# Optimization experiments

Hardware: AMD Instinct MI355X
Metric: run time of the kernel (lower is better)

The kernel has to match this reference:

```python
import jax, jax.numpy as jnp
import numpy as np

N_NODES = 50000
N_EDGES = 1_600_000
NFEAT = 512
NHID = 256  # nhid*2 = 512, nhid*3 = 768
NCLASS = 64
H2, H3 = 2 * NHID, 3 * NHID


def _uniform(key, shape, stdv):
    return jax.random.uniform(key, shape, jnp.float32, -stdv, stdv)


def setup_inputs() -> dict:
    key = jax.random.key(0)
    ks = jax.random.split(key, 16)
    x = jax.random.normal(ks[0], (N_NODES, NFEAT), jnp.float32)
    adj_row = jax.random.randint(ks[1], (N_EDGES,), 0, N_NODES, jnp.int64 if jax.config.jax_enable_x64 else jnp.int32)
    adj_col = jax.random.randint(ks[2], (N_EDGES,), 0, N_NODES, jnp.int64 if jax.config.jax_enable_x64 else jnp.int32)
    adj_val = jax.random.uniform(ks[3], (N_EDGES,), jnp.float32)
    # nn.Linear init: U(-1/sqrt(fan_in), 1/sqrt(fan_in)); GraphConvolution: U(-1/sqrt(out), 1/sqrt(out))
    s_org = 1.0 / np.sqrt(NFEAT)
    s_gc1 = 1.0 / np.sqrt(H3)
    s_gc2 = 1.0 / np.sqrt(H3)
    s_l3 = 1.0 / np.sqrt(H2)
    s_out = 1.0 / np.sqrt(H3)
    return {
        "x": x, "adj_row": adj_row, "adj_col": adj_col, "adj_val": adj_val,
        "W_org": _uniform(ks[4], (NFEAT, H2), s_org), "b_org": _uniform(ks[5], (H2,), s_org),
        "W_gc1": _uniform(ks[6], (H2, H3), s_gc1), "b_gc1": _uniform(ks[7], (H3,), s_gc1),
        "W_gc2": _uniform(ks[8], (H3, H3), s_gc2), "b_gc2": _uniform(ks[9], (H3,), s_gc2),
        "W_l3": _uniform(ks[10], (H2, H3), s_l3), "b_l3": _uniform(ks[11], (H3,), s_l3),
        "W_out": _uniform(ks[12], (H3, NCLASS), s_out), "b_out": _uniform(ks[13], (NCLASS,), s_out),
    }


def _spmm(row, col, val, dense):
    # out[i] = sum_{e: row[e]==i} val[e] * dense[col[e]]
    msgs = val[:, None] * dense[col]            # [E, F] gather + scale
    return jax.ops.segment_sum(msgs, row, num_segments=N_NODES)


def reference(x, adj_row, adj_col, adj_val,
              W_org, b_org, W_gc1, b_gc1, W_gc2, b_gc2,
              W_l3, b_l3, W_out, b_out):
    # linear_org (dropout = identity in eval)
    h = x @ W_org + b_org                       # [N, H2]
    # GCN layer 1: mm then spmm, bias, relu
    g = _spmm(adj_row, adj_col, adj_val, h @ W_gc1) + b_gc1
    g = jax.nn.relu(g)
    # GCN layer 2
    g = _spmm(adj_row, adj_col, adj_val, g @ W_gc2) + b_gc2
    # residual mix + output head
    z = (h @ W_l3 + b_l3) + 0.5 * g             # [N, H3]
    out = z @ W_out + b_out                     # [N, NCLASS]
    # global min-max normalization to [-1, 1]
    mn, mx = jnp.min(out), jnp.max(out)
    return 2.0 * (out - mn) / (mx - mn) - 1.0
```

## Files before the change

kernel.cpp:

```cpp
#include <hip/hip_runtime.h>

#define N_NODES 50000
#define N_EDGES 1600000
#define NFEAT   512
#define H2      512
#define H3      768
#define NCLASS  64
#define E_CAP   (N_EDGES + 8 * N_NODES)

typedef __attribute__((ext_vector_type(8))) short bf16x8;
typedef __attribute__((ext_vector_type(4))) float f32x4;
typedef __attribute__((ext_vector_type(8))) _Float16 f16x8;
typedef __attribute__((ext_vector_type(8))) unsigned short u16x8;

__device__ __forceinline__ unsigned short f2bf(float f) {
    unsigned u = __builtin_bit_cast(unsigned, f);
    unsigned r = (u + 0x7FFF + ((u >> 16) & 1)) >> 16;
    return (unsigned short)r;
}
__device__ __forceinline__ float bf2f(unsigned short h) {
    unsigned u = ((unsigned)h) << 16;
    return __builtin_bit_cast(float, u);
}

__device__ __forceinline__ void gload_lds16(const void* g, void* l) {
    __builtin_amdgcn_global_load_lds(
        (const __attribute__((address_space(1))) void*)g,
        (__attribute__((address_space(3))) void*)l, 16, 0, 0);
}

__global__ __launch_bounds__(256) void fold_weights_kernel(
    const float* __restrict__ Wgc2, const float* __restrict__ Wl3,
    const float* __restrict__ Wout, const float* __restrict__ b_gc2,
    const float* __restrict__ b_l3, const float* __restrict__ b_out,
    float* __restrict__ Wco, float* __restrict__ Wlo, float* __restrict__ bias_total)
{
    const int b = blockIdx.x;
    const int tid = threadIdx.x;
    if (b < 192) {
        int elem = b * 256 + tid;
        int r = elem >> 6, c = elem & 63;
        float s = 0.f;
        for (int k = 0; k < H3; ++k)
            s = fmaf(Wgc2[r * H3 + k], Wout[k * NCLASS + c], s);
        Wco[elem] = s;
    } else if (b < 320) {
        int elem = (b - 192) * 256 + tid;
        int r = elem >> 6, c = elem & 63;
        float s = 0.f;
        for (int k = 0; k < H3; ++k)
            s = fmaf(Wl3[r * H3 + k], Wout[k * NCLASS + c], s);
        Wlo[elem] = s;
    } else {
        if (tid < NCLASS) {
            float s = b_out[tid];
            for (int k = 0; k < H3; ++k)
                s = fmaf(b_l3[k] + 0.5f * b_gc2[k], Wout[k * NCLASS + tid], s);
            bias_total[tid] = s;
        }
    }
}

__global__ __launch_bounds__(256) void prep_weights_kernel(
    const float* __restrict__ Worg, const float* __restrict__ Wgc1,
    const float* __restrict__ Wco, const float* __restrict__ Wlo,
    unsigned short* __restrict__ WorgT_hi, unsigned short* __restrict__ WorgT_lo,
    unsigned short* __restrict__ Wgc1T_hi, unsigned short* __restrict__ Wgc1T_lo,
    unsigned short* __restrict__ WcoT_hi,  unsigned short* __restrict__ WcoT_lo,
    unsigned short* __restrict__ WloT_hi,  unsigned short* __restrict__ WloT_lo)
{
    int e = blockIdx.x * 256 + threadIdx.x;
    float v; unsigned short* hi; unsigned short* lo; int idx;
    if (e < 262144) {
        int n = e >> 9, k = e & 511;
        v = Worg[k * H2 + n]; hi = WorgT_hi; lo = WorgT_lo; idx = e;
    } else if (e < 262144 + 393216) {
        int e2 = e - 262144;
        int n = e2 >> 9, k = e2 & 511;
        v = Wgc1[k * H3 + n]; hi = Wgc1T_hi; lo = Wgc1T_lo; idx = e2;
    } else if (e < 262144 + 393216 + 49152) {
        int e3 = e - 262144 - 393216;
        int n = e3 / H3, k = e3 % H3;
        v = Wco[k * NCLASS + n]; hi = WcoT_hi; lo = WcoT_lo; idx = e3;
    } else if (e < 262144 + 393216 + 49152 + 32768) {
        int e4 = e - 262144 - 393216 - 49152;
        int n = e4 >> 9, k = e4 & 511;
        v = Wlo[k * NCLASS + n]; hi = WloT_hi; lo = WloT_lo; idx = e4;
    } else return;
    unsigned short hv = f2bf(v);
    hi[idx] = hv;
    lo[idx] = f2bf(v - bf2f(hv));
}

__global__ __launch_bounds__(256) void hist_kernel(const int* __restrict__ rows,
                                                   int* __restrict__ counts)
{
    int e = blockIdx.x * 256 + threadIdx.x;
    if (e < N_EDGES) atomicAdd(&counts[rows[e]], 1);
}

__global__ __launch_bounds__(256) void scan_blocks_kernel(
    const int* __restrict__ counts, int* __restrict__ row_ptr,
    int* __restrict__ btot, int n)
{
    __shared__ int wsum[4];
    const int idx = blockIdx.x * 256 + threadIdx.x;
    const int lane = threadIdx.x & 63;
    const int wid  = threadIdx.x >> 6;
    int v = (idx < n) ? ((counts[idx] + 7) & ~7) : 0;
    int x = v;
    #pragma unroll
    for (int off = 1; off < 64; off <<= 1) {
        int y = __shfl_up(x, off, 64);
        if (lane >= off) x += y;
    }
    if (lane == 63) wsum[wid] = x;
    __syncthreads();
    if (threadIdx.x == 0) {
        int s = 0;
        #pragma unroll
        for (int i = 0; i < 4; ++i) { int t = wsum[i]; wsum[i] = s; s += t; }
        btot[blockIdx.x] = s;
    }
    __syncthreads();
    if (idx < n) row_ptr[idx] = x - v + wsum[wid];
}

__global__ __launch_bounds__(256) void scan_tots_kernel(int* __restrict__ btot, int nb)
{
    __shared__ int wsum[4];
    const int tid = threadIdx.x;
    const int lane = tid & 63;
    const int wid  = tid >> 6;
    int v = (tid < nb) ? btot[tid] : 0;
    int x = v;
    #pragma unroll
    for (int off = 1; off < 64; off <<= 1) {
        int y = __shfl_up(x, off, 64);
        if (lane >= off) x += y;
    }
    if (lane == 63) wsum[wid] = x;
    __syncthreads();
    if (tid == 0) {
        int s = 0;
        #pragma unroll
        for (int i = 0; i < 4; ++i) { int t = wsum[i]; wsum[i] = s; s += t; }
    }
    __syncthreads();
    int excl = x - v + wsum[wid];
    if (tid < nb) btot[tid] = excl;
    if (tid == nb - 1) btot[nb] = excl + v;
}

__global__ __launch_bounds__(256) void scan_add_kernel(
    const int* __restrict__ btot, int* __restrict__ row_ptr,
    int* __restrict__ row_cur, int n)
{
    int idx = blockIdx.x * 256 + threadIdx.x;
    if (idx < n) {
        int o = row_ptr[idx] + btot[blockIdx.x];
        row_ptr[idx] = o;
        row_cur[idx] = o;
    }
    if (idx == 0) row_ptr[n] = btot[gridDim.x];
}

__global__ __launch_bounds__(256) void scatter_kernel(
    const int* __restrict__ rows, const int* __restrict__ cols,
    const float* __restrict__ vals, int* __restrict__ row_cur,
    int* __restrict__ cols_s, float* __restrict__ vals_s)
{
    int e = blockIdx.x * 256 + threadIdx.x;
    if (e < N_EDGES) {
        int r = rows[e];
        int p = atomicAdd(&row_cur[r], 1);
        cols_s[p] = cols[e];
        vals_s[p] = vals[e];
    }
}

template <int BN, int EPI, int AMODE, int WMODE>
__global__ __launch_bounds__(256, 2) void gemm_mfma(
    const float* __restrict__ Af, const _Float16* __restrict__ Ah16,
    const unsigned short* __restrict__ Ahi, const unsigned short* __restrict__ Alo,
    const unsigned short* __restrict__ Bhi, const unsigned short* __restrict__ Blo,
    const float* __restrict__ bias, const float* __restrict__ extra,
    float* __restrict__ Cf, _Float16* __restrict__ Ch16,
    unsigned short* __restrict__ Chi, unsigned short* __restrict__ Clo,
    int M, int N, int K, int NB)
{
    constexpr int WNF = BN / 32;
    constexpr int BF  = BN / 16;
    constexpr int NCH = 16 + 2 * BF;
    __shared__ unsigned short lds[NCH * 512];

    const int tid  = threadIdx.x;
    const int lane = tid & 63;
    const int wid  = tid >> 6;
    const int wr   = wid >> 1, wc = wid & 1;
    const int fr   = lane & 15;
    const int fk   = (lane >> 4) * 8;

    const int nwg = gridDim.x;
    const int u = blockIdx.x;
    const int q = nwg >> 3, r = nwg & 7;
    const int xcd = u & 7, pos = u >> 3;
    const int wg = (xcd < r ? xcd * (q + 1) : r * (q + 1) + (xcd - r) * q) + pos;
    const int m0 = (wg / NB) * 128;
    const int n0 = (wg % NB) * BN;

    f32x4 acc[4][WNF];
    #pragma unroll
    for (int mi = 0; mi < 4; ++mi)
        #pragma unroll
        for (int ni = 0; ni < WNF; ++ni)
            acc[mi][ni] = (f32x4){0.f, 0.f, 0.f, 0.f};

    for (int kt = 0; kt < K; kt += 32) {
        if constexpr (AMODE != 0) {
            #pragma unroll
            for (int sub = wid; sub < 8; sub += 4) {
                int row = m0 + sub * 16 + fr;
                if (row >= M) row = M - 1;
                float v[8];
                if constexpr (AMODE == 1) {
                    const float* src = Af + (size_t)row * K + kt + fk;
                    float4 p0 = *(const float4*)src;
                    float4 p1 = *(const float4*)(src + 4);
                    v[0] = p0.x; v[1] = p0.y; v[2] = p0.z; v[3] = p0.w;
                    v[4] = p1.x; v[5] = p1.y; v[6] = p1.z; v[7] = p1.w;
                } else {
                    const _Float16* src = Ah16 + (size_t)row * K + kt + fk;
                    f16x8 p = *(const f16x8*)src;
                    #pragma unroll
                    for (int j = 0; j < 8; ++j) v[j] = (float)p[j];
                }
                bf16x8 h8, l8;
                #pragma unroll
                for (int j = 0; j < 8; ++j) {
                    unsigned short hv = f2bf(v[j]);
                    h8[j] = (short)hv;
                    l8[j] = (short)f2bf(v[j] - bf2f(hv));
                }
                *(bf16x8*)&lds[sub * 512 + lane * 8] = h8;
                *(bf16x8*)&lds[(8 + sub) * 512 + lane * 8] = l8;
            }
            for (int ch = 16 + wid; ch < NCH; ch += 4) {
                int bch = ch - 16;
                int sub = bch % BF;
                const unsigned short* base = (bch < BF) ? Bhi : Blo;
                int col = n0 + sub * 16 + fr;
                gload_lds16(base + (size_t)col * K + kt + fk, &lds[ch * 512]);
            }
        } else {
            for (int ch = wid; ch < NCH; ch += 4) {
                const unsigned short* src;
                if (ch < 16) {
                    int sub = ch & 7;
                    int row = m0 + sub * 16 + fr;
                    if (row >= M) row = M - 1;
                    const unsigned short* base = (ch < 8) ? Ahi : Alo;
                    src = base + (size_t)row * K + kt + fk;
                } else {
                    int bch = ch - 16;
                    int sub = bch % BF;
                    const unsigned short* base = (bch < BF) ? Bhi : Blo;
                    int col = n0 + sub * 16 + fr;
                    src = base + (size_t)col * K + kt + fk;
                }
                gload_lds16(src, &lds[ch * 512]);
            }
        }
        __syncthreads();

        bf16x8 ah[4], al[4], bh[WNF], bl[WNF];
        #pragma unroll
        for (int mi = 0; mi < 4; ++mi) {
            int mf = wr * 4 + mi;
            ah[mi] = *(const bf16x8*)&lds[mf * 512 + lane * 8];
            al[mi] = *(const bf16x8*)&lds[(8 + mf) * 512 + lane * 8];
        }
        #pragma unroll
        for (int ni = 0; ni < WNF; ++ni) {
            int nf = wc * WNF + ni;
            bh[ni] = *(const bf16x8*)&lds[(16 + nf) * 512 + lane * 8];
            bl[ni] = *(const bf16x8*)&lds[(16 + BF + nf) * 512 + lane * 8];
        }
        #pragma unroll
        for (int mi = 0; mi < 4; ++mi)
            #pragma unroll
            for (int ni = 0; ni < WNF; ++ni) {
                acc[mi][ni] = __builtin_amdgcn_mfma_f32_16x16x32_bf16(
                    ah[mi], bh[ni], acc[mi][ni], 0, 0, 0);
                acc[mi][ni] = __builtin_amdgcn_mfma_f32_16x16x32_bf16(
                    ah[mi], bl[ni], acc[mi][ni], 0, 0, 0);
                acc[mi][ni] = __builtin_amdgcn_mfma_f32_16x16x32_bf16(
                    al[mi], bh[ni], acc[mi][ni], 0, 0, 0);
            }
        __syncthreads();
    }

    const int r0 = m0 + wr * 64 + (lane >> 4) * 4;
    const int c0 = n0 + wc * (BN / 2) + (lane & 15);
    #pragma unroll
    for (int mi = 0; mi < 4; ++mi)
        #pragma unroll
        for (int ni = 0; ni < WNF; ++ni) {
            int col = c0 + ni * 16;
            float bv = 0.f;
            if constexpr (EPI > 0) bv = bias[col];
            #pragma unroll
            for (int qi = 0; qi < 4; ++qi) {
                int row = r0 + mi * 16 + qi;
                if (row >= M) continue;
                float v = acc[mi][ni][qi] + bv;
                if constexpr (EPI == 2) v = fmaxf(v, 0.f);
                if constexpr (EPI == 3)
                    v = fmaf(0.5f, extra[(size_t)row * N + col], v);
                size_t idx = (size_t)row * N + col;
                if constexpr (WMODE == 0) Cf[idx] = v;
                if constexpr (WMODE == 1) {
                    unsigned short hv = f2bf(v);
                    Chi[idx] = hv;
                    Clo[idx] = f2bf(v - bf2f(hv));
                }
                if constexpr (WMODE == 2) Ch16[idx] = (_Float16)v;
            }
        }
}

__global__ __launch_bounds__(256) void spmm_csr512_f16(
    const int* __restrict__ row_ptr, const int* __restrict__ cols,
    const float* __restrict__ vals, const _Float16* __restrict__ dense,
    unsigned short* __restrict__ out_hi, unsigned short* __restrict__ out_lo)
{
    const int row = blockIdx.x * 4 + (threadIdx.x >> 6);
    const int c8 = (threadIdx.x & 63) * 8;
    int e = row_ptr[row];
    const int e1 = row_ptr[row + 1];
    float acc[8] = {0.f, 0.f, 0.f, 0.f, 0.f, 0.f, 0.f, 0.f};
    for (; e < e1; e += 8) {
        int4   ca = *(const int4*)&cols[e];
        int4   cb = *(const int4*)&cols[e + 4];
        float4 va = *(const float4*)&vals[e];
        float4 vb = *(const float4*)&vals[e + 4];
        f16x8 d0 = *(const f16x8*)&dense[(size_t)ca.x * 512 + c8];
        f16x8 d1 = *(const f16x8*)&dense[(size_t)ca.y * 512 + c8];
        f16x8 d2 = *(const f16x8*)&dense[(size_t)ca.z * 512 + c8];
        f16x8 d3 = *(const f16x8*)&dense[(size_t)ca.w * 512 + c8];
        f16x8 d4 = *(const f16x8*)&dense[(size_t)cb.x * 512 + c8];
        f16x8 d5 = *(const f16x8*)&dense[(size_t)cb.y * 512 + c8];
        f16x8 d6 = *(const f16x8*)&dense[(size_t)cb.z * 512 + c8];
        f16x8 d7 = *(const f16x8*)&dense[(size_t)cb.w * 512 + c8];
        #pragma unroll
        for (int j = 0; j < 8; ++j) {
            float a = acc[j];
            a = fmaf(va.x, (float)d0[j], a);
            a = fmaf(va.y, (float)d1[j], a);
            a = fmaf(va.z, (float)d2[j], a);
            a = fmaf(va.w, (float)d3[j], a);
            a = fmaf(vb.x, (float)d4[j], a);
            a = fmaf(vb.y, (float)d5[j], a);
            a = fmaf(vb.z, (float)d6[j], a);
            a = fmaf(vb.w, (float)d7[j], a);
            acc[j] = a;
        }
    }
    u16x8 h8, l8;
    #pragma unroll
    for (int j = 0; j < 8; ++j) {
        unsigned short hv = f2bf(acc[j]);
        h8[j] = hv;
        l8[j] = f2bf(acc[j] - bf2f(hv));
    }
    *(u16x8*)&out_hi[(size_t)row * 512 + c8] = h8;
    *(u16x8*)&out_lo[(size_t)row * 512 + c8] = l8;
}

__global__ __launch_bounds__(256) void spmm_csr64(
    const int* __restrict__ row_ptr, const int* __restrict__ cols,
    const float* __restrict__ vals, const float* __restrict__ dense,
    float* __restrict__ out)
{
    const int row = blockIdx.x * 4 + (threadIdx.x >> 6);
    const int c = threadIdx.x & 63;
    int e = row_ptr[row];
    const int e1 = row_ptr[row + 1];
    float a0 = 0.f, a1 = 0.f, a2 = 0.f, a3 = 0.f;
    for (; e < e1; e += 4) {
        int c0 = cols[e], c1 = cols[e + 1], c2 = cols[e + 2], c3 = cols[e + 3];
        float v0 = vals[e], v1 = vals[e + 1], v2 = vals[e + 2], v3 = vals[e + 3];
        a0 = fmaf(v0, dense[(size_t)c0 * 64 + c], a0);
        a1 = fmaf(v1, dense[(size_t)c1 * 64 + c], a1);
        a2 = fmaf(v2, dense[(size_t)c2 * 64 + c], a2);
        a3 = fmaf(v3, dense[(size_t)c3 * 64 + c], a3);
    }
    out[(size_t)row * 64 + c] = (a0 + a1) + (a2 + a3);
}

__global__ __launch_bounds__(256) void minmax_partial(const float* __restrict__ x,
                                                      int n, float* __restrict__ part)
{
    float mn = 3.4e38f, mx = -3.4e38f;
    for (int i = blockIdx.x * 256 + threadIdx.x; i < n; i += gridDim.x * 256) {
        float v = x[i];
        mn = fminf(mn, v); mx = fmaxf(mx, v);
    }
    #pragma unroll
    for (int off = 32; off > 0; off >>= 1) {
        mn = fminf(mn, __shfl_down(mn, off, 64));
        mx = fmaxf(mx, __shfl_down(mx, off, 64));
    }
    __shared__ float smn[4], smx[4];
    if ((threadIdx.x & 63) == 0) { smn[threadIdx.x >> 6] = mn; smx[threadIdx.x >> 6] = mx; }
    __syncthreads();
    if (threadIdx.x == 0) {
        mn = fminf(fminf(smn[0], smn[1]), fminf(smn[2], smn[3]));
        mx = fmaxf(fmaxf(smx[0], smx[1]), fmaxf(smx[2], smx[3]));
        part[blockIdx.x] = mn;
        part[gridDim.x + blockIdx.x] = mx;
    }
}

__global__ __launch_bounds__(256) void minmax_final(const float* __restrict__ part,
                                                    float* __restrict__ mm)
{
    float mn = part[threadIdx.x], mx = part[256 + threadIdx.x];
    #pragma unroll
    for (int off = 32; off > 0; off >>= 1) {
        mn = fminf(mn, __shfl_down(mn, off, 64));
        mx = fmaxf(mx, __shfl_down(mx, off, 64));
    }
    __shared__ float smn[4], smx[4];
    if ((threadIdx.x & 63) == 0) { smn[threadIdx.x >> 6] = mn; smx[threadIdx.x >> 6] = mx; }
    __syncthreads();
    if (threadIdx.x == 0) {
        mm[0] = fminf(fminf(smn[0], smn[1]), fminf(smn[2], smn[3]));
        mm[1] = fmaxf(fmaxf(smx[0], smx[1]), fmaxf(smx[2], smx[3]));
    }
}

__global__ __launch_bounds__(256) void normalize_kernel(float4* __restrict__ x, int n4,
                                                        const float* __restrict__ mm)
{
    int i = blockIdx.x * 256 + threadIdx.x;
    if (i >= n4) return;
    float mn = mm[0];
    float s = 2.0f / (mm[1] - mn);
    float4 v = x[i];
    v.x = fmaf(v.x - mn, s, -1.f);
    v.y = fmaf(v.y - mn, s, -1.f);
    v.z = fmaf(v.z - mn, s, -1.f);
    v.w = fmaf(v.w - mn, s, -1.f);
    x[i] = v;
}

extern "C" void kernel_launch(void* const* d_in, const int* in_sizes, int n_in,
                              void* d_out, int out_size, void* d_ws, size_t ws_size,
                              hipStream_t stream)
{
    const float* x       = (const float*)d_in[0];
    const int*   adj_row = (const int*)d_in[1];
    const int*   adj_col = (const int*)d_in[2];
    const float* adj_val = (const float*)d_in[3];
    const float* W_org = (const float*)d_in[4];
    const float* b_org = (const float*)d_in[5];
    const float* W_gc1 = (const float*)d_in[6];
    const float* b_gc1 = (const float*)d_in[7];
    const float* W_gc2 = (const float*)d_in[8];
    const float* b_gc2 = (const float*)d_in[9];
    const float* W_l3  = (const float*)d_in[10];
    const float* b_l3  = (const float*)d_in[11];
    const float* W_out = (const float*)d_in[12];
    const float* b_out = (const float*)d_in[13];
    float* out = (float*)d_out;

    char* w = (char*)d_ws;
    size_t off = 0;
    auto alloc = [&](size_t bytes) -> void* {
        void* p = w + off;
        off += (bytes + 255) & ~(size_t)255;
        return p;
    };
    unsigned short* g_hi = (unsigned short*)alloc((size_t)N_NODES * H3 * 2);
    unsigned short* g_lo = (unsigned short*)alloc((size_t)N_NODES * H3 * 2);
    _Float16* h16 = (_Float16*)alloc((size_t)N_NODES * H2 * 2);
    char* region_ah = (char*)alloc((size_t)N_NODES * H2 * 4);
    unsigned short* ah_hi = (unsigned short*)region_ah;
    unsigned short* ah_lo = ah_hi + (size_t)N_NODES * H2;
    float* s   = (float*)region_ah;
    float* as_ = s + (size_t)N_NODES * NCLASS;
    int*   counts  = (int*)alloc((size_t)N_NODES * 4);
    int*   row_ptr = (int*)alloc((size_t)(N_NODES + 1) * 4);
    int*   row_cur = (int*)alloc((size_t)N_NODES * 4);
    int*   btot    = (int*)alloc(256 * 4);
    int*   cols_s  = (int*)alloc((size_t)E_CAP * 4);
    float* vals_s  = (float*)alloc((size_t)E_CAP * 4);
    float* Wco = (float*)alloc((size_t)H3 * NCLASS * 4);
    float* Wlo = (float*)alloc((size_t)H2 * NCLASS * 4);
    unsigned short* WorgT_hi = (unsigned short*)alloc((size_t)H2 * NFEAT * 2);
    unsigned short* WorgT_lo = (unsigned short*)alloc((size_t)H2 * NFEAT * 2);
    unsigned short* Wgc1T_hi = (unsigned short*)alloc((size_t)H3 * H2 * 2);
    unsigned short* Wgc1T_lo = (unsigned short*)alloc((size_t)H3 * H2 * 2);
    unsigned short* WcoT_hi  = (unsigned short*)alloc((size_t)NCLASS * H3 * 2);
    unsigned short* WcoT_lo  = (unsigned short*)alloc((size_t)NCLASS * H3 * 2);
    unsigned short* WloT_hi  = (unsigned short*)alloc((size_t)NCLASS * H2 * 2);
    unsigned short* WloT_lo  = (unsigned short*)alloc((size_t)NCLASS * H2 * 2);
    float* bias_total = (float*)alloc(NCLASS * 4);
    float* part = (float*)alloc(512 * 4);
    float* mm   = (float*)alloc(2 * 4);
    (void)ws_size; (void)n_in; (void)in_sizes; (void)out_size;

    hipMemsetAsync(counts, 0, (size_t)N_NODES * 4, stream);
    hipMemsetAsync(cols_s, 0, (size_t)E_CAP * 4, stream);
    hipMemsetAsync(vals_s, 0, (size_t)E_CAP * 4, stream);
    fold_weights_kernel<<<321, 256, 0, stream>>>(W_gc2, W_l3, W_out, b_gc2, b_l3,
                                                 b_out, Wco, Wlo, bias_total);
    prep_weights_kernel<<<2880, 256, 0, stream>>>(W_org, W_gc1, Wco, Wlo,
        WorgT_hi, WorgT_lo, Wgc1T_hi, Wgc1T_lo, WcoT_hi, WcoT_lo, WloT_hi, WloT_lo);
    hist_kernel<<<N_EDGES / 256, 256, 0, stream>>>(adj_row, counts);
    const int NSB = (N_NODES + 255) / 256;
    scan_blocks_kernel<<<NSB, 256, 0, stream>>>(counts, row_ptr, btot, N_NODES);
    scan_tots_kernel<<<1, 256, 0, stream>>>(btot, NSB);
    scan_add_kernel<<<NSB, 256, 0, stream>>>(btot, row_ptr, row_cur, N_NODES);
    scatter_kernel<<<N_EDGES / 256, 256, 0, stream>>>(adj_row, adj_col, adj_val,
                                                      row_cur, cols_s, vals_s);

    const int MB = (N_NODES + 127) / 128;

    gemm_mfma<128, 1, 1, 2><<<MB * 4, 256, 0, stream>>>(
        x, nullptr, nullptr, nullptr, WorgT_hi, WorgT_lo, b_org, nullptr,
        nullptr, h16, nullptr, nullptr, N_NODES, H2, NFEAT, 4);
    spmm_csr512_f16<<<N_NODES / 4, 256, 0, stream>>>(row_ptr, cols_s, vals_s, h16,
                                                     ah_hi, ah_lo);
    gemm_mfma<128, 2, 0, 1><<<MB * 6, 256, 0, stream>>>(
        nullptr, nullptr, ah_hi, ah_lo, Wgc1T_hi, Wgc1T_lo, b_gc1, nullptr,
        nullptr, nullptr, g_hi, g_lo, N_NODES, H3, H2, 6);
    gemm_mfma<64, 0, 0, 0><<<MB, 256, 0, stream>>>(
        nullptr, nullptr, g_hi, g_lo, WcoT_hi, WcoT_lo, nullptr, nullptr,
        s, nullptr, nullptr, nullptr, N_NODES, NCLASS, H3, 1);
    spmm_csr64<<<N_NODES / 4, 256, 0, stream>>>(row_ptr, cols_s, vals_s, s, as_);
    gemm_mfma<64, 3, 2, 0><<<MB, 256, 0, stream>>>(
        nullptr, h16, nullptr, nullptr, WloT_hi, WloT_lo, bias_total, as_,
        out, nullptr, nullptr, nullptr, N_NODES, NCLASS, H2, 1);

    const int n_out = N_NODES * NCLASS;
    minmax_partial<<<256, 256, 0, stream>>>(out, n_out, part);
    minmax_final<<<1, 256, 0, stream>>>(part, mm);
    normalize_kernel<<<(n_out / 4 + 255) / 256, 256, 0, stream>>>(
        (float4*)out, n_out / 4, mm);
}
```

Measured before the change: 1.133 ms.

## Replace split-bf16 three-MFMA GEMMs with single fp16 MFMA and fp16 intermediates

```diff
diff --git a/kernel.cpp b/kernel.cpp
--- a/kernel.cpp
+++ b/kernel.cpp
@@ -8,20 +8,8 @@
 #define NCLASS  64
 #define E_CAP   (N_EDGES + 8 * N_NODES)
 
-typedef __attribute__((ext_vector_type(8))) short bf16x8;
 typedef __attribute__((ext_vector_type(4))) float f32x4;
 typedef __attribute__((ext_vector_type(8))) _Float16 f16x8;
-typedef __attribute__((ext_vector_type(8))) unsigned short u16x8;
-
-__device__ __forceinline__ unsigned short f2bf(float f) {
-    unsigned u = __builtin_bit_cast(unsigned, f);
-    unsigned r = (u + 0x7FFF + ((u >> 16) & 1)) >> 16;
-    return (unsigned short)r;
-}
-__device__ __forceinline__ float bf2f(unsigned short h) {
-    unsigned u = ((unsigned)h) << 16;
-    return __builtin_bit_cast(float, u);
-}
 
 __device__ __forceinline__ void gload_lds16(const void* g, void* l) {
     __builtin_amdgcn_global_load_lds(
@@ -61,35 +49,44 @@
     }
 }
 
-__global__ __launch_bounds__(256) void prep_weights_kernel(
+__global__ __launch_bounds__(256) void prep_weights_f16(
     const float* __restrict__ Worg, const float* __restrict__ Wgc1,
     const float* __restrict__ Wco, const float* __restrict__ Wlo,
-    unsigned short* __restrict__ WorgT_hi, unsigned short* __restrict__ WorgT_lo,
-    unsigned short* __restrict__ Wgc1T_hi, unsigned short* __restrict__ Wgc1T_lo,
-    unsigned short* __restrict__ WcoT_hi,  unsigned short* __restrict__ WcoT_lo,
-    unsigned short* __restrict__ WloT_hi,  unsigned short* __restrict__ WloT_lo)
+    _Float16* __restrict__ WorgT, _Float16* __restrict__ Wgc1T,
+    _Float16* __restrict__ WcoT,  _Float16* __restrict__ WloT)
 {
     int e = blockIdx.x * 256 + threadIdx.x;
-    float v; unsigned short* hi; unsigned short* lo; int idx;
     if (e < 262144) {
         int n = e >> 9, k = e & 511;
-        v = Worg[k * H2 + n]; hi = WorgT_hi; lo = WorgT_lo; idx = e;
+        WorgT[e] = (_Float16)Worg[k * H2 + n];
     } else if (e < 262144 + 393216) {
         int e2 = e - 262144;
         int n = e2 >> 9, k = e2 & 511;
-        v = Wgc1[k * H3 + n]; hi = Wgc1T_hi; lo = Wgc1T_lo; idx = e2;
+        Wgc1T[e2] = (_Float16)Wgc1[k * H3 + n];
     } else if (e < 262144 + 393216 + 49152) {
         int e3 = e - 262144 - 393216;
         int n = e3 / H3, k = e3 % H3;
-        v = Wco[k * NCLASS + n]; hi = WcoT_hi; lo = WcoT_lo; idx = e3;
+        WcoT[e3] = (_Float16)Wco[k * NCLASS + n];
     } else if (e < 262144 + 393216 + 49152 + 32768) {
         int e4 = e - 262144 - 393216 - 49152;
         int n = e4 >> 9, k = e4 & 511;
-        v = Wlo[k * NCLASS + n]; hi = WloT_hi; lo = WloT_lo; idx = e4;
-    } else return;
-    unsigned short hv = f2bf(v);
-    hi[idx] = hv;
-    lo[idx] = f2bf(v - bf2f(hv));
+        WloT[e4] = (_Float16)Wlo[k * NCLASS + n];
+    }
+}
+
+__global__ __launch_bounds__(256) void convert_x_kernel(
+    const float* __restrict__ x, _Float16* __restrict__ x16, int n8)
+{
+    int i = blockIdx.x * 256 + threadIdx.x;
+    if (i >= n8) return;
+    const float4* src = (const float4*)&x[i * 8];
+    float4 a = src[0], b = src[1];
+    f16x8 o;
+    o[0] = (_Float16)a.x; o[1] = (_Float16)a.y;
+    o[2] = (_Float16)a.z; o[3] = (_Float16)a.w;
+    o[4] = (_Float16)b.x; o[5] = (_Float16)b.y;
+    o[6] = (_Float16)b.z; o[7] = (_Float16)b.w;
+    *(f16x8*)&x16[i * 8] = o;
 }
 
 __global__ __launch_bounds__(256) void hist_kernel(const int* __restrict__ rows,
@@ -179,20 +176,17 @@
     }
 }
 
-template <int BN, int EPI, int AMODE, int WMODE>
-__global__ __launch_bounds__(256, 2) void gemm_mfma(
-    const float* __restrict__ Af, const _Float16* __restrict__ Ah16,
-    const unsigned short* __restrict__ Ahi, const unsigned short* __restrict__ Alo,
-    const unsigned short* __restrict__ Bhi, const unsigned short* __restrict__ Blo,
+template <int BN, int EPI, int WMODE>
+__global__ __launch_bounds__(256, 2) void gemm_f16(
+    const _Float16* __restrict__ A16, const _Float16* __restrict__ B16,
     const float* __restrict__ bias, const float* __restrict__ extra,
     float* __restrict__ Cf, _Float16* __restrict__ Ch16,
-    unsigned short* __restrict__ Chi, unsigned short* __restrict__ Clo,
     int M, int N, int K, int NB)
 {
     constexpr int WNF = BN / 32;
     constexpr int BF  = BN / 16;
-    constexpr int NCH = 16 + 2 * BF;
-    __shared__ unsigned short lds[NCH * 512];
+    constexpr int NCH = 8 + BF;
+    __shared__ _Float16 lds[NCH * 512];
 
     const int tid  = threadIdx.x;
     const int lane = tid & 63;
@@ -217,86 +211,33 @@
             acc[mi][ni] = (f32x4){0.f, 0.f, 0.f, 0.f};
 
     for (int kt = 0; kt < K; kt += 32) {
-        if constexpr (AMODE != 0) {
-            #pragma unroll
-            for (int sub = wid; sub < 8; sub += 4) {
-                int row = m0 + sub * 16 + fr;
+        for (int ch = wid; ch < NCH; ch += 4) {
+            const _Float16* src;
+            if (ch < 8) {
+                int row = m0 + ch * 16 + fr;
                 if (row >= M) row = M - 1;
-                float v[8];
-                if constexpr (AMODE == 1) {
-                    const float* src = Af + (size_t)row * K + kt + fk;
-                    float4 p0 = *(const float4*)src;
-                    float4 p1 = *(const float4*)(src + 4);
-                    v[0] = p0.x; v[1] = p0.y; v[2] = p0.z; v[3] = p0.w;
-                    v[4] = p1.x; v[5] = p1.y; v[6] = p1.z; v[7] = p1.w;
-                } else {
-                    const _Float16* src = Ah16 + (size_t)row * K + kt + fk;
-                    f16x8 p = *(const f16x8*)src;
-                    #pragma unroll
-                    for (int j = 0; j < 8; ++j) v[j] = (float)p[j];
-                }
-                bf16x8 h8, l8;
-                #pragma unroll
-                for (int j = 0; j < 8; ++j) {
-                    unsigned short hv = f2bf(v[j]);
-                    h8[j] = (short)hv;
-                    l8[j] = (short)f2bf(v[j] - bf2f(hv));
-                }
-                *(bf16x8*)&lds[sub * 512 + lane * 8] = h8;
-                *(bf16x8*)&lds[(8 + sub) * 512 + lane * 8] = l8;
+                src = A16 + (size_t)row * K + kt + fk;
+            } else {
+                int col = n0 + (ch - 8) * 16 + fr;
+                src = B16 + (size_t)col * K + kt + fk;
             }
-            for (int ch = 16 + wid; ch < NCH; ch += 4) {
-                int bch = ch - 16;
-                int sub = bch % BF;
-                const unsigned short* base = (bch < BF) ? Bhi : Blo;
-                int col = n0 + sub * 16 + fr;
-                gload_lds16(base + (size_t)col * K + kt + fk, &lds[ch * 512]);
-            }
-        } else {
-            for (int ch = wid; ch < NCH; ch += 4) {
-                const unsigned short* src;
-                if (ch < 16) {
-                    int sub = ch & 7;
-                    int row = m0 + sub * 16 + fr;
-                    if (row >= M) row = M - 1;
-                    const unsigned short* base = (ch < 8) ? Ahi : Alo;
-                    src = base + (size_t)row * K + kt + fk;
-                } else {
-                    int bch = ch - 16;
-                    int sub = bch % BF;
-                    const unsigned short* base = (bch < BF) ? Bhi : Blo;
-                    int col = n0 + sub * 16 + fr;
-                    src = base + (size_t)col * K + kt + fk;
-                }
-                gload_lds16(src, &lds[ch * 512]);
-            }
+            gload_lds16(src, &lds[ch * 512]);
         }
         __syncthreads();
 
-        bf16x8 ah[4], al[4], bh[WNF], bl[WNF];
-        #pragma unroll
-        for (int mi = 0; mi < 4; ++mi) {
-            int mf = wr * 4 + mi;
-            ah[mi] = *(const bf16x8*)&lds[mf * 512 + lane * 8];
-            al[mi] = *(const bf16x8*)&lds[(8 + mf) * 512 + lane * 8];
-        }
-        #pragma unroll
-        for (int ni = 0; ni < WNF; ++ni) {
-            int nf = wc * WNF + ni;
-            bh[ni] = *(const bf16x8*)&lds[(16 + nf) * 512 + lane * 8];
-            bl[ni] = *(const bf16x8*)&lds[(16 + BF + nf) * 512 + lane * 8];
-        }
+        f16x8 a[4], b[WNF];
+        #pragma unroll
+        for (int mi = 0; mi < 4; ++mi)
+            a[mi] = *(const f16x8*)&lds[(wr * 4 + mi) * 512 + lane * 8];
+        #pragma unroll
+        for (int ni = 0; ni < WNF; ++ni)
+            b[ni] = *(const f16x8*)&lds[(8 + wc * WNF + ni) * 512 + lane * 8];
         #pragma unroll
         for (int mi = 0; mi < 4; ++mi)
             #pragma unroll
-            for (int ni = 0; ni < WNF; ++ni) {
-                acc[mi][ni] = __builtin_amdgcn_mfma_f32_16x16x32_bf16(
-                    ah[mi], bh[ni], acc[mi][ni], 0, 0, 0);
-                acc[mi][ni] = __builtin_amdgcn_mfma_f32_16x16x32_bf16(
-                    ah[mi], bl[ni], acc[mi][ni], 0, 0, 0);
-                acc[mi][ni] = __builtin_amdgcn_mfma_f32_16x16x32_bf16(
-                    al[mi], bh[ni], acc[mi][ni], 0, 0, 0);
-            }
+            for (int ni = 0; ni < WNF; ++ni)
+                acc[mi][ni] = __builtin_amdgcn_mfma_f32_16x16x32_f16(
+                    a[mi], b[ni], acc[mi][ni], 0, 0, 0);
         __syncthreads();
     }
 
@@ -319,11 +260,6 @@
                     v = fmaf(0.5f, extra[(size_t)row * N + col], v);
                 size_t idx = (size_t)row * N + col;
                 if constexpr (WMODE == 0) Cf[idx] = v;
-                if constexpr (WMODE == 1) {
-                    unsigned short hv = f2bf(v);
-                    Chi[idx] = hv;
-                    Clo[idx] = f2bf(v - bf2f(hv));
-                }
                 if constexpr (WMODE == 2) Ch16[idx] = (_Float16)v;
             }
         }
@@ -332,7 +268,7 @@
 __global__ __launch_bounds__(256) void spmm_csr512_f16(
     const int* __restrict__ row_ptr, const int* __restrict__ cols,
     const float* __restrict__ vals, const _Float16* __restrict__ dense,
-    unsigned short* __restrict__ out_hi, unsigned short* __restrict__ out_lo)
+    _Float16* __restrict__ out16)
 {
     const int row = blockIdx.x * 4 + (threadIdx.x >> 6);
     const int c8 = (threadIdx.x & 63) * 8;
@@ -366,20 +302,15 @@
             acc[j] = a;
         }
     }
-    u16x8 h8, l8;
-    #pragma unroll
-    for (int j = 0; j < 8; ++j) {
-        unsigned short hv = f2bf(acc[j]);
-        h8[j] = hv;
-        l8[j] = f2bf(acc[j] - bf2f(hv));
-    }
-    *(u16x8*)&out_hi[(size_t)row * 512 + c8] = h8;
-    *(u16x8*)&out_lo[(size_t)row * 512 + c8] = l8;
-}
-
-__global__ __launch_bounds__(256) void spmm_csr64(
+    f16x8 o;
+    #pragma unroll
+    for (int j = 0; j < 8; ++j) o[j] = (_Float16)acc[j];
+    *(f16x8*)&out16[(size_t)row * 512 + c8] = o;
+}
+
+__global__ __launch_bounds__(256) void spmm_csr64_f16(
     const int* __restrict__ row_ptr, const int* __restrict__ cols,
-    const float* __restrict__ vals, const float* __restrict__ dense,
+    const float* __restrict__ vals, const _Float16* __restrict__ dense,
     float* __restrict__ out)
 {
     const int row = blockIdx.x * 4 + (threadIdx.x >> 6);
@@ -390,10 +321,10 @@
     for (; e < e1; e += 4) {
         int c0 = cols[e], c1 = cols[e + 1], c2 = cols[e + 2], c3 = cols[e + 3];
         float v0 = vals[e], v1 = vals[e + 1], v2 = vals[e + 2], v3 = vals[e + 3];
-        a0 = fmaf(v0, dense[(size_t)c0 * 64 + c], a0);
-        a1 = fmaf(v1, dense[(size_t)c1 * 64 + c], a1);
-        a2 = fmaf(v2, dense[(size_t)c2 * 64 + c], a2);
-        a3 = fmaf(v3, dense[(size_t)c3 * 64 + c], a3);
+        a0 = fmaf(v0, (float)dense[(size_t)c0 * 64 + c], a0);
+        a1 = fmaf(v1, (float)dense[(size_t)c1 * 64 + c], a1);
+        a2 = fmaf(v2, (float)dense[(size_t)c2 * 64 + c], a2);
+        a3 = fmaf(v3, (float)dense[(size_t)c3 * 64 + c], a3);
     }
     out[(size_t)row * 64 + c] = (a0 + a1) + (a2 + a3);
 }
@@ -482,14 +413,12 @@
         off += (bytes + 255) & ~(size_t)255;
         return p;
     };
-    unsigned short* g_hi = (unsigned short*)alloc((size_t)N_NODES * H3 * 2);
-    unsigned short* g_lo = (unsigned short*)alloc((size_t)N_NODES * H3 * 2);
-    _Float16* h16 = (_Float16*)alloc((size_t)N_NODES * H2 * 2);
-    char* region_ah = (char*)alloc((size_t)N_NODES * H2 * 4);
-    unsigned short* ah_hi = (unsigned short*)region_ah;
-    unsigned short* ah_lo = ah_hi + (size_t)N_NODES * H2;
-    float* s   = (float*)region_ah;
-    float* as_ = s + (size_t)N_NODES * NCLASS;
+    _Float16* g16  = (_Float16*)alloc((size_t)N_NODES * H3 * 2);
+    _Float16* h16  = (_Float16*)alloc((size_t)N_NODES * H2 * 2);
+    _Float16* ah16 = (_Float16*)alloc((size_t)N_NODES * H2 * 2);
+    _Float16* x16  = (_Float16*)alloc((size_t)N_NODES * NFEAT * 2);
+    _Float16* s16  = (_Float16*)alloc((size_t)N_NODES * NCLASS * 2);
+    float*    as_  = (float*)alloc((size_t)N_NODES * NCLASS * 4);
     int*   counts  = (int*)alloc((size_t)N_NODES * 4);
     int*   row_ptr = (int*)alloc((size_t)(N_NODES + 1) * 4);
     int*   row_cur = (int*)alloc((size_t)N_NODES * 4);
@@ -498,14 +427,10 @@
     float* vals_s  = (float*)alloc((size_t)E_CAP * 4);
     float* Wco = (float*)alloc((size_t)H3 * NCLASS * 4);
     float* Wlo = (float*)alloc((size_t)H2 * NCLASS * 4);
-    unsigned short* WorgT_hi = (unsigned short*)alloc((size_t)H2 * NFEAT * 2);
-    unsigned short* WorgT_lo = (unsigned short*)alloc((size_t)H2 * NFEAT * 2);
-    unsigned short* Wgc1T_hi = (unsigned short*)alloc((size_t)H3 * H2 * 2);
-    unsigned short* Wgc1T_lo = (unsigned short*)alloc((size_t)H3 * H2 * 2);
-    unsigned short* WcoT_hi  = (unsigned short*)alloc((size_t)NCLASS * H3 * 2);
-    unsigned short* WcoT_lo  = (unsigned short*)alloc((size_t)NCLASS * H3 * 2);
-    unsigned short* WloT_hi  = (unsigned short*)alloc((size_t)NCLASS * H2 * 2);
-    unsigned short* WloT_lo  = (unsigned short*)alloc((size_t)NCLASS * H2 * 2);
+    _Float16* WorgT = (_Float16*)alloc((size_t)H2 * NFEAT * 2);
+    _Float16* Wgc1T = (_Float16*)alloc((size_t)H3 * H2 * 2);
+    _Float16* WcoT  = (_Float16*)alloc((size_t)NCLASS * H3 * 2);
+    _Float16* WloT  = (_Float16*)alloc((size_t)NCLASS * H2 * 2);
     float* bias_total = (float*)alloc(NCLASS * 4);
     float* part = (float*)alloc(512 * 4);
     float* mm   = (float*)alloc(2 * 4);
@@ -516,8 +441,10 @@
     hipMemsetAsync(vals_s, 0, (size_t)E_CAP * 4, stream);
     fold_weights_kernel<<<321, 256, 0, stream>>>(W_gc2, W_l3, W_out, b_gc2, b_l3,
                                                  b_out, Wco, Wlo, bias_total);
-    prep_weights_kernel<<<2880, 256, 0, stream>>>(W_org, W_gc1, Wco, Wlo,
-        WorgT_hi, WorgT_lo, Wgc1T_hi, Wgc1T_lo, WcoT_hi, WcoT_lo, WloT_hi, WloT_lo);
+    prep_weights_f16<<<2880, 256, 0, stream>>>(W_org, W_gc1, Wco, Wlo,
+                                               WorgT, Wgc1T, WcoT, WloT);
+    convert_x_kernel<<<(N_NODES * NFEAT / 8 + 255) / 256, 256, 0, stream>>>(
+        x, x16, N_NODES * NFEAT / 8);
     hist_kernel<<<N_EDGES / 256, 256, 0, stream>>>(adj_row, counts);
     const int NSB = (N_NODES + 255) / 256;
     scan_blocks_kernel<<<NSB, 256, 0, stream>>>(counts, row_ptr, btot, N_NODES);
@@ -528,21 +455,18 @@
 
     const int MB = (N_NODES + 127) / 128;
 
-    gemm_mfma<128, 1, 1, 2><<<MB * 4, 256, 0, stream>>>(
-        x, nullptr, nullptr, nullptr, WorgT_hi, WorgT_lo, b_org, nullptr,
-        nullptr, h16, nullptr, nullptr, N_NODES, H2, NFEAT, 4);
-    spmm_csr512_f16<<<N_NODES / 4, 256, 0, stream>>>(row_ptr, cols_s, vals_s, h16,
-                                                     ah_hi, ah_lo);
-    gemm_mfma<128, 2, 0, 1><<<MB * 6, 256, 0, stream>>>(
-        nullptr, nullptr, ah_hi, ah_lo, Wgc1T_hi, Wgc1T_lo, b_gc1, nullptr,
-        nullptr, nullptr, g_hi, g_lo, N_NODES, H3, H2, 6);
-    gemm_mfma<64, 0, 0, 0><<<MB, 256, 0, stream>>>(
-        nullptr, nullptr, g_hi, g_lo, WcoT_hi, WcoT_lo, nullptr, nullptr,
-        s, nullptr, nullptr, nullptr, N_NODES, NCLASS, H3, 1);
-    spmm_csr64<<<N_NODES / 4, 256, 0, stream>>>(row_ptr, cols_s, vals_s, s, as_);
-    gemm_mfma<64, 3, 2, 0><<<MB, 256, 0, stream>>>(
-        nullptr, h16, nullptr, nullptr, WloT_hi, WloT_lo, bias_total, as_,
-        out, nullptr, nullptr, nullptr, N_NODES, NCLASS, H2, 1);
+    gemm_f16<128, 1, 2><<<MB * 4, 256, 0, stream>>>(
+        x16, WorgT, b_org, nullptr, nullptr, h16, N_NODES, H2, NFEAT, 4);
+    spmm_csr512_f16<<<N_NODES / 4, 256, 0, stream>>>(row_ptr, cols_s, vals_s,
+                                                     h16, ah16);
+    gemm_f16<128, 2, 2><<<MB * 6, 256, 0, stream>>>(
+        ah16, Wgc1T, b_gc1, nullptr, nullptr, g16, N_NODES, H3, H2, 6);
+    gemm_f16<64, 0, 2><<<MB, 256, 0, stream>>>(
+        g16, WcoT, nullptr, nullptr, nullptr, s16, N_NODES, NCLASS, H3, 1);
+    spmm_csr64_f16<<<N_NODES / 4, 256, 0, stream>>>(row_ptr, cols_s, vals_s,
+                                                    s16, as_);
+    gemm_f16<64, 3, 0><<<MB, 256, 0, stream>>>(
+        h16, WloT, bias_total, as_, out, nullptr, N_NODES, NCLASS, H2, 1);
 
     const int n_out = N_NODES * NCLASS;
     minmax_partial<<<256, 256, 0, stream>>>(out, n_out, part);
```

New measurement: 917.5 us. 19.0% less time.
